# Kernel tuning notes

Measured on AMD Instinct MI355X. Metric: run time of the kernel, lower is better.

## Reference

```python
import jax, jax.numpy as jnp
import numpy as np

B, NI, NO = 4, 256, 256          # batch, num_in, num_out
DIN, DQ, DH, DOUT = 256, 256, 256, 256


def setup_inputs() -> dict:
    key = jax.random.key(0)
    ks = jax.random.split(key, 6)
    def w(k, shape, fan_in):
        return jax.random.normal(k, shape, jnp.float32) / np.sqrt(fan_in).astype(np.float32)
    return {
        "x": jax.random.normal(ks[0], (B, NI, DIN), jnp.float32),
        "query": jax.random.normal(ks[1], (B, NO, DQ), jnp.float32),
        # pre_cond_mlp: Linear(DIN -> DH)
        "W_pre": w(ks[2], (DIN, DH), DIN), "b_pre": jnp.zeros((DH,), jnp.float32),
        # cond_embed: Linear(DQ -> DH)
        "W_emb": w(ks[3], (DQ, DH), DQ), "b_emb": jnp.zeros((DH,), jnp.float32),
        # post_cond_mlp: Linear(2*DH -> DH) + GELU + Linear(DH -> DOUT)
        "W1": w(ks[4], (2 * DH, DH), 2 * DH), "b1": jnp.zeros((DH,), jnp.float32),
        "W2": w(ks[5], (DH, DOUT), DH), "b2": jnp.zeros((DOUT,), jnp.float32),
    }


def reference(x, query, W_pre, b_pre, W_emb, b_emb, W1, b1, W2, b2):
    # pre_cond_mlp(x): [B, NI, DH]
    xp = x @ W_pre + b_pre
    # cond_embed(query): [B, NO, DH]
    c = query @ W_emb + b_emb
    # Original torch code: repeat xp over NO, c over NI, concat -> [B,NI,NO,2*DH],
    # then Linear(2*DH->DH). Algebraically identical (and far cheaper) to split W1
    # and broadcast-add the two projections:
    W1x, W1c = W1[:DH], W1[DH:]          # [DH, DH] each
    h = (xp @ W1x)[:, :, None, :] + (c @ W1c)[:, None, :, :] + b1  # [B, NI, NO, DH]
    h = jax.nn.gelu(h, approximate=False)  # torch nn.GELU default = exact erf
    return h @ W2 + b2                     # [B, NI, NO, DOUT]
```

## Files before the change

### kernel.cpp

```cpp
#include <hip/hip_runtime.h>
#include <hip/hip_bf16.h>
#include <cstdint>
#include <cstddef>


typedef __bf16  bf16x8 __attribute__((ext_vector_type(8)));
typedef float   f32x16 __attribute__((ext_vector_type(16)));

__device__ __forceinline__ float fast_gelu(float x) {
    const float x2 = x * x;
    const float m  = __builtin_fmaf(x2, -0.1029433f, -2.3022072f);
    const float e  = __builtin_amdgcn_exp2f(x * m);
    return x * __builtin_amdgcn_rcpf(1.0f + e);
}

__global__ __launch_bounds__(256) void prep_kernel(
    const float* __restrict__ x, const float* __restrict__ query,
    const float* __restrict__ W_pre, const float* __restrict__ b_pre,
    const float* __restrict__ W_emb, const float* __restrict__ b_emb,
    const float* __restrict__ W1, const float* __restrict__ b1,
    const float* __restrict__ W2,
    float* __restrict__ u, float* __restrict__ v,
    unsigned short* __restrict__ w2t)
{
    const int b = blockIdx.x;
    const int t = threadIdx.x;

    if (b >= 512) {
        const int n0 = (b - 512) * 4;
        const float4 wv = *reinterpret_cast<const float4*>(W2 + (size_t)t * 256 + n0);
        const float vals[4] = {wv.x, wv.y, wv.z, wv.w};
#pragma unroll
        for (int j = 0; j < 4; ++j) {
            const __bf16 bv = (__bf16)vals[j];
            w2t[(size_t)(n0 + j) * 256 + t] = __builtin_bit_cast(unsigned short, bv);
        }
        return;
    }

    const bool isq = (b >= 256);
    const float* __restrict__ A   = isq ? query : x;
    const float* __restrict__ Wa  = isq ? W_emb : W_pre;
    const float* __restrict__ ba  = isq ? b_emb : b_pre;
    const float* __restrict__ W1p = isq ? (W1 + 256 * 256) : W1;
    float* __restrict__ outp      = isq ? v : u;
    const int r0 = (isq ? (b - 256) : b) * 4;

    __shared__ float as[4][256];
    __shared__ float xs[4][256];

#pragma unroll
    for (int r = 0; r < 4; ++r)
        as[r][t] = A[(size_t)(r0 + r) * 256 + t];
    __syncthreads();

    float acc[4] = {0.f, 0.f, 0.f, 0.f};
    {
        float wcur[8];
#pragma unroll
        for (int q = 0; q < 8; ++q) wcur[q] = Wa[(size_t)q * 256 + t];
        for (int k0 = 0; k0 < 248; k0 += 8) {
            float wnxt[8];
#pragma unroll
            for (int q = 0; q < 8; ++q)
                wnxt[q] = Wa[(size_t)(k0 + 8 + q) * 256 + t];
#pragma unroll
            for (int q = 0; q < 8; ++q)
#pragma unroll
                for (int r = 0; r < 4; ++r)
                    acc[r] = __builtin_fmaf(as[r][k0 + q], wcur[q], acc[r]);
#pragma unroll
            for (int q = 0; q < 8; ++q) wcur[q] = wnxt[q];
        }
#pragma unroll
        for (int q = 0; q < 8; ++q)
#pragma unroll
            for (int r = 0; r < 4; ++r)
                acc[r] = __builtin_fmaf(as[r][248 + q], wcur[q], acc[r]);
    }
    const float bav = ba[t];
#pragma unroll
    for (int r = 0; r < 4; ++r) xs[r][t] = acc[r] + bav;
    __syncthreads();

    float acc2[4] = {0.f, 0.f, 0.f, 0.f};
    {
        float wcur[8];
#pragma unroll
        for (int q = 0; q < 8; ++q) wcur[q] = W1p[(size_t)q * 256 + t];
        for (int k0 = 0; k0 < 248; k0 += 8) {
            float wnxt[8];
#pragma unroll
            for (int q = 0; q < 8; ++q)
                wnxt[q] = W1p[(size_t)(k0 + 8 + q) * 256 + t];
#pragma unroll
            for (int q = 0; q < 8; ++q)
#pragma unroll
                for (int r = 0; r < 4; ++r)
                    acc2[r] = __builtin_fmaf(xs[r][k0 + q], wcur[q], acc2[r]);
#pragma unroll
            for (int q = 0; q < 8; ++q) wcur[q] = wnxt[q];
        }
#pragma unroll
        for (int q = 0; q < 8; ++q)
#pragma unroll
            for (int r = 0; r < 4; ++r)
                acc2[r] = __builtin_fmaf(xs[r][248 + q], wcur[q], acc2[r]);
    }
    const float b1v = isq ? 0.f : b1[t];
#pragma unroll
    for (int r = 0; r < 4; ++r)
        outp[(size_t)(r0 + r) * 256 + t] = acc2[r] + b1v;
}

__global__ __launch_bounds__(256, 2) void fused_kernel(
    const float* __restrict__ U, const float* __restrict__ V,
    const unsigned short* __restrict__ W2T, const float* __restrict__ b2,
    float* __restrict__ out)
{
    __shared__ uint4 wlds[2048];
    __shared__ uint4 hlds[1024];
    unsigned int* const hlds32 = reinterpret_cast<unsigned int*>(hlds);

    const int t    = threadIdx.x;
    const int lane = t & 63;
    const int w    = t >> 6;
    const int l31  = lane & 31;
    const int hi   = lane >> 5;

    const size_t r0 = (size_t)blockIdx.x * 128;
    const int bb = (int)(r0 >> 16);
    const int ii = (int)((r0 >> 8) & 255);
    const int j0 = (int)(r0 & 255);

    const float* __restrict__ urow  = U + ((size_t)(bb * 256 + ii)) * 256;
    const float* __restrict__ vbase = V + ((size_t)(bb * 256 + j0)) * 256;

    f32x16 acc[8];
#pragma unroll
    for (int i = 0; i < 8; ++i) acc[i] = (f32x16)0.f;

    for (int kk = 0; kk < 256; kk += 64) {
#pragma unroll
        for (int it = 0; it < 8; ++it) {
            const int idx = it * 256 + t;
            const int n   = idx >> 3;
            const int gp  = idx & 7;
            const int g   = gp ^ (n & 7);
            __builtin_amdgcn_global_load_lds(
                (const __attribute__((address_space(1))) unsigned int*)
                    (W2T + (size_t)n * 256 + kk + g * 8),
                (__attribute__((address_space(3))) unsigned int*)
                    (wlds + idx),
                16, 0, 0);
        }

        const float2 uv2 = *reinterpret_cast<const float2*>(urow + kk + 2 * l31);
        float2 vv[16];
#pragma unroll
        for (int p = 0; p < 16; ++p) {
            const int row = w * 32 + p * 2 + hi;
            vv[p] = *reinterpret_cast<const float2*>(vbase + (size_t)row * 256 + kk + 2 * l31);
        }
#pragma unroll
        for (int p = 0; p < 16; ++p) {
            const int row = w * 32 + p * 2 + hi;
            union { unsigned int u32; __bf16 h[2]; } pk;
            pk.h[0] = (__bf16)fast_gelu(uv2.x + vv[p].x);
            pk.h[1] = (__bf16)fast_gelu(uv2.y + vv[p].y);
            const int d = l31;
            hlds32[row * 32 + (((d >> 2) ^ (row & 7)) << 2) + (d & 3)] = pk.u32;
        }
        __syncthreads();

#pragma unroll
        for (int s = 0; s < 4; ++s) {
            const int gk = 2 * s + hi;
            const int arow = w * 32 + l31;
            const bf16x8 afrag = __builtin_bit_cast(
                bf16x8, hlds[arow * 8 + (gk ^ (arow & 7))]);
#pragma unroll
            for (int cg = 0; cg < 8; ++cg) {
                const int col = cg * 32 + l31;
                const bf16x8 bfrag = __builtin_bit_cast(
                    bf16x8, wlds[col * 8 + (gk ^ (col & 7))]);
                acc[cg] = __builtin_amdgcn_mfma_f32_32x32x16_bf16(
                    afrag, bfrag, acc[cg], 0, 0, 0);
            }
        }
        __syncthreads();
    }

#pragma unroll
    for (int cg = 0; cg < 8; ++cg) {
        const int col = cg * 32 + l31;
        const float bv = b2[col];
#pragma unroll
        for (int rr = 0; rr < 16; ++rr) {
            const int row = w * 32 + 4 * hi + (rr & 3) + 8 * (rr >> 2);
            __builtin_nontemporal_store(acc[cg][rr] + bv,
                                        out + (r0 + row) * 256 + col);
        }
    }
}

extern "C" void kernel_launch(void* const* d_in, const int* in_sizes, int n_in,
                              void* d_out, int out_size, void* d_ws, size_t ws_size,
                              hipStream_t stream)
{
    const float* x     = (const float*)d_in[0];
    const float* query = (const float*)d_in[1];
    const float* W_pre = (const float*)d_in[2];
    const float* b_pre = (const float*)d_in[3];
    const float* W_emb = (const float*)d_in[4];
    const float* b_emb = (const float*)d_in[5];
    const float* W1    = (const float*)d_in[6];
    const float* b1    = (const float*)d_in[7];
    const float* W2    = (const float*)d_in[8];
    const float* b2    = (const float*)d_in[9];
    float* out = (float*)d_out;

    char* ws = (char*)d_ws;
    float* u            = (float*)(ws);
    float* v            = (float*)(ws + (1 << 20));
    unsigned short* w2t = (unsigned short*)(ws + 2 * (1 << 20));

    prep_kernel<<<576, 256, 0, stream>>>(x, query, W_pre, b_pre, W_emb, b_emb,
                                         W1, b1, W2, u, v, w2t);
    fused_kernel<<<2048, 256, 0, stream>>>(u, v, w2t, b2, out);
}
```

Baseline: 105.1 us.

## Keep half of W2 resident in LDS and loop over tasks in persistent blocks

The fused kernel now launches 512 blocks, each owning one 128-column half of W2. That half, covering all K, is loaded into LDS once. Each block then loops over 8 row tiles, with register double-buffering of the U/V loads across K chunks and across tasks. Per-chunk block barriers are dropped because each wave writes and reads only its own rows of the GELU tile. This removes repeated W2 streaming and barrier stalls, but every GELU element is now computed twice (once per column half), LDS use grows, and fewer blocks are resident.

```diff
diff --git a/kernel.cpp b/kernel.cpp
--- a/kernel.cpp
+++ b/kernel.cpp
@@ -118,88 +118,135 @@
     const unsigned short* __restrict__ W2T, const float* __restrict__ b2,
     float* __restrict__ out)
 {
-    __shared__ uint4 wlds[2048];
+    __shared__ uint4 wlds[4096];
     __shared__ uint4 hlds[1024];
-    unsigned int* const hlds32 = reinterpret_cast<unsigned int*>(hlds);
+    unsigned int* const h32 = reinterpret_cast<unsigned int*>(hlds);
 
     const int t    = threadIdx.x;
     const int lane = t & 63;
     const int w    = t >> 6;
     const int l31  = lane & 31;
     const int hi   = lane >> 5;
-
-    const size_t r0 = (size_t)blockIdx.x * 128;
-    const int bb = (int)(r0 >> 16);
-    const int ii = (int)((r0 >> 8) & 255);
-    const int j0 = (int)(r0 & 255);
-
-    const float* __restrict__ urow  = U + ((size_t)(bb * 256 + ii)) * 256;
-    const float* __restrict__ vbase = V + ((size_t)(bb * 256 + j0)) * 256;
-
-    f32x16 acc[8];
-#pragma unroll
-    for (int i = 0; i < 8; ++i) acc[i] = (f32x16)0.f;
-
-    for (int kk = 0; kk < 256; kk += 64) {
-#pragma unroll
-        for (int it = 0; it < 8; ++it) {
-            const int idx = it * 256 + t;
-            const int n   = idx >> 3;
-            const int gp  = idx & 7;
-            const int g   = gp ^ (n & 7);
-            __builtin_amdgcn_global_load_lds(
-                (const __attribute__((address_space(1))) unsigned int*)
-                    (W2T + (size_t)n * 256 + kk + g * 8),
-                (__attribute__((address_space(3))) unsigned int*)
-                    (wlds + idx),
-                16, 0, 0);
-        }
-
-        const float2 uv2 = *reinterpret_cast<const float2*>(urow + kk + 2 * l31);
-        float2 vv[16];
+    const int d    = l31;
+
+    const int bid = blockIdx.x;
+    const int ch  = bid & 1;
+    const int grp = bid >> 1;
+    const int n0  = ch * 128;
+
+#pragma unroll
+    for (int it = 0; it < 16; ++it) {
+        const int idx = it * 256 + t;
+        const int n   = idx >> 5;
+        const int gp  = idx & 31;
+        const int g   = (gp & 24) | ((gp ^ n) & 7);
+        __builtin_amdgcn_global_load_lds(
+            (const __attribute__((address_space(1))) unsigned int*)
+                (W2T + (size_t)(n0 + n) * 256 + g * 8),
+            (__attribute__((address_space(3))) unsigned int*)(wlds + idx),
+            16, 0, 0);
+    }
+
+    float bvv[4];
+#pragma unroll
+    for (int cg = 0; cg < 4; ++cg) bvv[cg] = b2[n0 + cg * 32 + l31];
+
+    float2 vvA[16], vvB[16];
+    float2 u2A, u2B;
+    const float* urow;
+    const float* vrow;
+
+    auto task_ptrs = [&](int task) {
+        const int P    = grp * 8 + task;
+        const int tile = P >> 1;
+        const int jh   = P & 1;
+        const int bb   = tile >> 8;
+        urow = U + (size_t)tile * 256;
+        vrow = V + ((size_t)(bb * 256 + jh * 128)) * 256;
+    };
+
+    auto load_t = [&](int kk, float2& u2, float2 (&vv)[16]) {
+        u2 = *reinterpret_cast<const float2*>(urow + kk + 2 * d);
 #pragma unroll
         for (int p = 0; p < 16; ++p) {
             const int row = w * 32 + p * 2 + hi;
-            vv[p] = *reinterpret_cast<const float2*>(vbase + (size_t)row * 256 + kk + 2 * l31);
-        }
+            vv[p] = *reinterpret_cast<const float2*>(
+                vrow + (size_t)row * 256 + kk + 2 * d);
+        }
+    };
+
+    auto gelu_write = [&](const float2& u2, const float2 (&vv)[16]) {
 #pragma unroll
         for (int p = 0; p < 16; ++p) {
             const int row = w * 32 + p * 2 + hi;
             union { unsigned int u32; __bf16 h[2]; } pk;
-            pk.h[0] = (__bf16)fast_gelu(uv2.x + vv[p].x);
-            pk.h[1] = (__bf16)fast_gelu(uv2.y + vv[p].y);
-            const int d = l31;
-            hlds32[row * 32 + (((d >> 2) ^ (row & 7)) << 2) + (d & 3)] = pk.u32;
-        }
-        __syncthreads();
-
+            pk.h[0] = (__bf16)fast_gelu(u2.x + vv[p].x);
+            pk.h[1] = (__bf16)fast_gelu(u2.y + vv[p].y);
+            h32[row * 32 + (((d >> 2) ^ (row & 7)) << 2) + (d & 3)] = pk.u32;
+        }
+    };
+
+    f32x16 acc[4];
+
+    auto mfma_chunk = [&](int kk) {
+        const int kg0 = kk >> 3;
 #pragma unroll
         for (int s = 0; s < 4; ++s) {
-            const int gk = 2 * s + hi;
+            const int gl   = 2 * s + hi;
             const int arow = w * 32 + l31;
             const bf16x8 afrag = __builtin_bit_cast(
-                bf16x8, hlds[arow * 8 + (gk ^ (arow & 7))]);
-#pragma unroll
-            for (int cg = 0; cg < 8; ++cg) {
-                const int col = cg * 32 + l31;
+                bf16x8, hlds[arow * 8 + (gl ^ (arow & 7))]);
+            const int gk = kg0 + gl;
+#pragma unroll
+            for (int cg = 0; cg < 4; ++cg) {
+                const int nloc = cg * 32 + l31;
+                const int slot = (gk & 24) | ((gk ^ nloc) & 7);
                 const bf16x8 bfrag = __builtin_bit_cast(
-                    bf16x8, wlds[col * 8 + (gk ^ (col & 7))]);
+                    bf16x8, wlds[nloc * 32 + slot]);
                 acc[cg] = __builtin_amdgcn_mfma_f32_32x32x16_bf16(
                     afrag, bfrag, acc[cg], 0, 0, 0);
             }
         }
-        __syncthreads();
-    }
-
-#pragma unroll
-    for (int cg = 0; cg < 8; ++cg) {
-        const int col = cg * 32 + l31;
-        const float bv = b2[col];
-#pragma unroll
-        for (int rr = 0; rr < 16; ++rr) {
-            const int row = w * 32 + 4 * hi + (rr & 3) + 8 * (rr >> 2);
-            __builtin_nontemporal_store(acc[cg][rr] + bv,
-                                        out + (r0 + row) * 256 + col);
+    };
+
+    task_ptrs(0);
+    load_t(0, u2A, vvA);
+
+    __syncthreads();
+
+    for (int task = 0; task < 8; ++task) {
+#pragma unroll
+        for (int i = 0; i < 4; ++i) acc[i] = (f32x16)0.f;
+
+        load_t(64, u2B, vvB);
+        gelu_write(u2A, vvA);
+        mfma_chunk(0);
+        load_t(128, u2A, vvA);
+        gelu_write(u2B, vvB);
+        mfma_chunk(64);
+        load_t(192, u2B, vvB);
+        gelu_write(u2A, vvA);
+        mfma_chunk(128);
+        const int P    = grp * 8 + task;
+        const int tile = P >> 1;
+        const int jh   = P & 1;
+        if (task < 7) {
+            task_ptrs(task + 1);
+            load_t(0, u2A, vvA);
+        }
+        gelu_write(u2B, vvB);
+        mfma_chunk(192);
+
+        const size_t obase = ((size_t)tile << 16) + (size_t)(jh * 128) * 256;
+#pragma unroll
+        for (int cg = 0; cg < 4; ++cg) {
+            const int col = n0 + cg * 32 + l31;
+#pragma unroll
+            for (int rr = 0; rr < 16; ++rr) {
+                const int row = w * 32 + 4 * hi + (rr & 3) + 8 * (rr >> 2);
+                __builtin_nontemporal_store(acc[cg][rr] + bvv[cg],
+                    out + obase + (size_t)row * 256 + col);
+            }
         }
     }
 }
@@ -227,5 +274,5 @@
 
     prep_kernel<<<576, 256, 0, stream>>>(x, query, W_pre, b_pre, W_emb, b_emb,
                                          W1, b1, W2, u, v, w2t);
-    fused_kernel<<<2048, 256, 0, stream>>>(u, v, w2t, b2, out);
-}
+    fused_kernel<<<512, 256, 0, stream>>>(u, v, w2t, b2, out);
+}
```

Result: slower. 112.1 us (+6.7%).

## Use 512-thread blocks with 2x2 wave tiling in fused GEMM kernel

Applied to the files above, without the earlier changes.

Doubles the block to eight waves arranged as a 2x2 grid of 64x64 output sub-tiles. This replaces four waves that each own a 32x256 strip. Each thread holds fewer MFMA accumulators, and the GELU/pack work is split across more threads in two passes. The aim is more resident waves per CU to hide store and load latency. In exchange, A fragments are reused less per B load and each block pays extra barrier cost.

```diff
diff --git a/kernel.cpp b/kernel.cpp
--- a/kernel.cpp
+++ b/kernel.cpp
@@ -113,20 +113,22 @@
         outp[(size_t)(r0 + r) * 256 + t] = acc2[r] + b1v;
 }
 
-__global__ __launch_bounds__(256, 2) void fused_kernel(
+__global__ __launch_bounds__(512, 4) void fused_kernel(
     const float* __restrict__ U, const float* __restrict__ V,
     const unsigned short* __restrict__ W2T, const float* __restrict__ b2,
     float* __restrict__ out)
 {
     __shared__ uint4 wlds[2048];
     __shared__ uint4 hlds[1024];
-    unsigned int* const hlds32 = reinterpret_cast<unsigned int*>(hlds);
+    unsigned int* const h32 = reinterpret_cast<unsigned int*>(hlds);
 
     const int t    = threadIdx.x;
     const int lane = t & 63;
     const int w    = t >> 6;
     const int l31  = lane & 31;
     const int hi   = lane >> 5;
+    const int wr   = w >> 2;
+    const int wc   = w & 3;
 
     const size_t r0 = (size_t)blockIdx.x * 128;
     const int bb = (int)(r0 >> 16);
@@ -136,70 +138,86 @@
     const float* __restrict__ urow  = U + ((size_t)(bb * 256 + ii)) * 256;
     const float* __restrict__ vbase = V + ((size_t)(bb * 256 + j0)) * 256;
 
-    f32x16 acc[8];
-#pragma unroll
-    for (int i = 0; i < 8; ++i) acc[i] = (f32x16)0.f;
+    const int d  = t & 31;
+    const int rb = t >> 5;
+
+    f32x16 acc[2][2];
+#pragma unroll
+    for (int rg = 0; rg < 2; ++rg)
+#pragma unroll
+        for (int cg = 0; cg < 2; ++cg) acc[rg][cg] = (f32x16)0.f;
 
     for (int kk = 0; kk < 256; kk += 64) {
 #pragma unroll
-        for (int it = 0; it < 8; ++it) {
-            const int idx = it * 256 + t;
+        for (int it = 0; it < 4; ++it) {
+            const int idx = it * 512 + t;
             const int n   = idx >> 3;
             const int gp  = idx & 7;
             const int g   = gp ^ (n & 7);
             __builtin_amdgcn_global_load_lds(
                 (const __attribute__((address_space(1))) unsigned int*)
                     (W2T + (size_t)n * 256 + kk + g * 8),
-                (__attribute__((address_space(3))) unsigned int*)
-                    (wlds + idx),
+                (__attribute__((address_space(3))) unsigned int*)(wlds + idx),
                 16, 0, 0);
         }
 
-        const float2 uv2 = *reinterpret_cast<const float2*>(urow + kk + 2 * l31);
-        float2 vv[16];
-#pragma unroll
-        for (int p = 0; p < 16; ++p) {
-            const int row = w * 32 + p * 2 + hi;
-            vv[p] = *reinterpret_cast<const float2*>(vbase + (size_t)row * 256 + kk + 2 * l31);
-        }
-#pragma unroll
-        for (int p = 0; p < 16; ++p) {
-            const int row = w * 32 + p * 2 + hi;
-            union { unsigned int u32; __bf16 h[2]; } pk;
-            pk.h[0] = (__bf16)fast_gelu(uv2.x + vv[p].x);
-            pk.h[1] = (__bf16)fast_gelu(uv2.y + vv[p].y);
-            const int d = l31;
-            hlds32[row * 32 + (((d >> 2) ^ (row & 7)) << 2) + (d & 3)] = pk.u32;
+        const float2 u2 = *reinterpret_cast<const float2*>(urow + kk + 2 * d);
+#pragma unroll 1
+        for (int pass = 0; pass < 2; ++pass) {
+            float2 vv[4];
+#pragma unroll
+            for (int p = 0; p < 4; ++p) {
+                const int row = rb + (pass * 4 + p) * 16;
+                vv[p] = *reinterpret_cast<const float2*>(
+                    vbase + (size_t)row * 256 + kk + 2 * d);
+            }
+#pragma unroll
+            for (int p = 0; p < 4; ++p) {
+                const int row = rb + (pass * 4 + p) * 16;
+                union { unsigned int u32; __bf16 h[2]; } pk;
+                pk.h[0] = (__bf16)fast_gelu(u2.x + vv[p].x);
+                pk.h[1] = (__bf16)fast_gelu(u2.y + vv[p].y);
+                h32[row * 32 + (((d >> 2) ^ (row & 7)) << 2) + (d & 3)] = pk.u32;
+            }
         }
         __syncthreads();
 
 #pragma unroll
         for (int s = 0; s < 4; ++s) {
             const int gk = 2 * s + hi;
-            const int arow = w * 32 + l31;
-            const bf16x8 afrag = __builtin_bit_cast(
-                bf16x8, hlds[arow * 8 + (gk ^ (arow & 7))]);
-#pragma unroll
-            for (int cg = 0; cg < 8; ++cg) {
-                const int col = cg * 32 + l31;
-                const bf16x8 bfrag = __builtin_bit_cast(
+            bf16x8 af[2];
+#pragma unroll
+            for (int rg = 0; rg < 2; ++rg) {
+                const int arow = wr * 64 + rg * 32 + l31;
+                af[rg] = __builtin_bit_cast(
+                    bf16x8, hlds[arow * 8 + (gk ^ (arow & 7))]);
+            }
+#pragma unroll
+            for (int cg = 0; cg < 2; ++cg) {
+                const int col = wc * 64 + cg * 32 + l31;
+                const bf16x8 bf_ = __builtin_bit_cast(
                     bf16x8, wlds[col * 8 + (gk ^ (col & 7))]);
-                acc[cg] = __builtin_amdgcn_mfma_f32_32x32x16_bf16(
-                    afrag, bfrag, acc[cg], 0, 0, 0);
+#pragma unroll
+                for (int rg = 0; rg < 2; ++rg)
+                    acc[rg][cg] = __builtin_amdgcn_mfma_f32_32x32x16_bf16(
+                        af[rg], bf_, acc[rg][cg], 0, 0, 0);
             }
         }
         __syncthreads();
     }
 
 #pragma unroll
-    for (int cg = 0; cg < 8; ++cg) {
-        const int col = cg * 32 + l31;
-        const float bv = b2[col];
-#pragma unroll
-        for (int rr = 0; rr < 16; ++rr) {
-            const int row = w * 32 + 4 * hi + (rr & 3) + 8 * (rr >> 2);
-            __builtin_nontemporal_store(acc[cg][rr] + bv,
-                                        out + (r0 + row) * 256 + col);
+    for (int rg = 0; rg < 2; ++rg) {
+#pragma unroll
+        for (int cg = 0; cg < 2; ++cg) {
+            const int col = wc * 64 + cg * 32 + l31;
+            const float bv = b2[col];
+#pragma unroll
+            for (int rr = 0; rr < 16; ++rr) {
+                const int row = wr * 64 + rg * 32 + 4 * hi + (rr & 3) + 8 * (rr >> 2);
+                __builtin_nontemporal_store(acc[rg][cg][rr] + bv,
+                                            out + (r0 + row) * 256 + col);
+            }
         }
     }
 }
@@ -227,5 +245,5 @@
 
     prep_kernel<<<576, 256, 0, stream>>>(x, query, W_pre, b_pre, W_emb, b_emb,
                                          W1, b1, W2, u, v, w2t);
-    fused_kernel<<<2048, 256, 0, stream>>>(u, v, w2t, b2, out);
-}
+    fused_kernel<<<2048, 512, 0, stream>>>(u, v, w2t, b2, out);
+}
```

Result: faster. 100.8 us (-4.0%).

## Drop LDS staging; build MFMA fragments directly from pre-transposed V and W2 layouts

Applied to the files above, without the earlier changes.

The prep kernel now writes V transposed and W2 in an MFMA-fragment-ready bf16 layout, so the fused kernel can build its A operand in registers from U plus strided V^T loads and read B fragments straight from global memory. This removes the shared-memory staging, swizzling and both barriers per k-step. Every wave now re-reads W2 fragments from global/L2 with no LDS reuse, and the V^T loads are strided per element. Nontemporal output stores are also replaced by plain stores.

```diff
diff --git a/kernel.cpp b/kernel.cpp
--- a/kernel.cpp
+++ b/kernel.cpp
@@ -20,8 +20,8 @@
     const float* __restrict__ W_emb, const float* __restrict__ b_emb,
     const float* __restrict__ W1, const float* __restrict__ b1,
     const float* __restrict__ W2,
-    float* __restrict__ u, float* __restrict__ v,
-    unsigned short* __restrict__ w2t)
+    float* __restrict__ u, float* __restrict__ vt,
+    unsigned short* __restrict__ w2f)
 {
     const int b = blockIdx.x;
     const int t = threadIdx.x;
@@ -30,10 +30,12 @@
         const int n0 = (b - 512) * 4;
         const float4 wv = *reinterpret_cast<const float4*>(W2 + (size_t)t * 256 + n0);
         const float vals[4] = {wv.x, wv.y, wv.z, wv.w};
+        const int g = t >> 3, e = t & 7;
 #pragma unroll
         for (int j = 0; j < 4; ++j) {
             const __bf16 bv = (__bf16)vals[j];
-            w2t[(size_t)(n0 + j) * 256 + t] = __builtin_bit_cast(unsigned short, bv);
+            w2f[((size_t)(g * 256 + n0 + j)) * 8 + e] =
+                __builtin_bit_cast(unsigned short, bv);
         }
         return;
     }
@@ -43,7 +45,6 @@
     const float* __restrict__ Wa  = isq ? W_emb : W_pre;
     const float* __restrict__ ba  = isq ? b_emb : b_pre;
     const float* __restrict__ W1p = isq ? (W1 + 256 * 256) : W1;
-    float* __restrict__ outp      = isq ? v : u;
     const int r0 = (isq ? (b - 256) : b) * 4;
 
     __shared__ float as[4][256];
@@ -107,99 +108,85 @@
             for (int r = 0; r < 4; ++r)
                 acc2[r] = __builtin_fmaf(xs[r][248 + q], wcur[q], acc2[r]);
     }
-    const float b1v = isq ? 0.f : b1[t];
-#pragma unroll
-    for (int r = 0; r < 4; ++r)
-        outp[(size_t)(r0 + r) * 256 + t] = acc2[r] + b1v;
+
+    if (!isq) {
+        const float b1v = b1[t];
+#pragma unroll
+        for (int r = 0; r < 4; ++r)
+            u[(size_t)(r0 + r) * 256 + t] = acc2[r] + b1v;
+    } else {
+        const int bb = r0 >> 8;
+        const int jb = r0 & 255;
+#pragma unroll
+        for (int r = 0; r < 4; ++r)
+            vt[((size_t)(bb * 256 + t)) * 256 + (jb + r)] = acc2[r];
+    }
 }
 
 __global__ __launch_bounds__(256, 2) void fused_kernel(
-    const float* __restrict__ U, const float* __restrict__ V,
-    const unsigned short* __restrict__ W2T, const float* __restrict__ b2,
+    const float* __restrict__ U, const float* __restrict__ VT,
+    const unsigned short* __restrict__ W2F, const float* __restrict__ b2,
     float* __restrict__ out)
 {
-    __shared__ uint4 wlds[2048];
-    __shared__ uint4 hlds[1024];
-    unsigned int* const hlds32 = reinterpret_cast<unsigned int*>(hlds);
-
     const int t    = threadIdx.x;
     const int lane = t & 63;
     const int w    = t >> 6;
     const int l31  = lane & 31;
     const int hi   = lane >> 5;
 
-    const size_t r0 = (size_t)blockIdx.x * 128;
-    const int bb = (int)(r0 >> 16);
-    const int ii = (int)((r0 >> 8) & 255);
-    const int j0 = (int)(r0 & 255);
-
-    const float* __restrict__ urow  = U + ((size_t)(bb * 256 + ii)) * 256;
-    const float* __restrict__ vbase = V + ((size_t)(bb * 256 + j0)) * 256;
+    const int bid  = blockIdx.x;
+    const int tile = bid >> 1;
+    const int jh   = bid & 1;
+    const int bb   = tile >> 8;
+
+    const int jloc = jh * 128 + w * 32 + l31;
+    const float* __restrict__ urow  = U + (size_t)tile * 256;
+    const float* __restrict__ vtcol = VT + ((size_t)(bb * 256)) * 256 + jloc;
 
     f32x16 acc[8];
 #pragma unroll
     for (int i = 0; i < 8; ++i) acc[i] = (f32x16)0.f;
 
-    for (int kk = 0; kk < 256; kk += 64) {
-#pragma unroll
-        for (int it = 0; it < 8; ++it) {
-            const int idx = it * 256 + t;
-            const int n   = idx >> 3;
-            const int gp  = idx & 7;
-            const int g   = gp ^ (n & 7);
-            __builtin_amdgcn_global_load_lds(
-                (const __attribute__((address_space(1))) unsigned int*)
-                    (W2T + (size_t)n * 256 + kk + g * 8),
-                (__attribute__((address_space(3))) unsigned int*)
-                    (wlds + idx),
-                16, 0, 0);
-        }
-
-        const float2 uv2 = *reinterpret_cast<const float2*>(urow + kk + 2 * l31);
-        float2 vv[16];
-#pragma unroll
-        for (int p = 0; p < 16; ++p) {
-            const int row = w * 32 + p * 2 + hi;
-            vv[p] = *reinterpret_cast<const float2*>(vbase + (size_t)row * 256 + kk + 2 * l31);
-        }
-#pragma unroll
-        for (int p = 0; p < 16; ++p) {
-            const int row = w * 32 + p * 2 + hi;
-            union { unsigned int u32; __bf16 h[2]; } pk;
-            pk.h[0] = (__bf16)fast_gelu(uv2.x + vv[p].x);
-            pk.h[1] = (__bf16)fast_gelu(uv2.y + vv[p].y);
-            const int d = l31;
-            hlds32[row * 32 + (((d >> 2) ^ (row & 7)) << 2) + (d & 3)] = pk.u32;
-        }
-        __syncthreads();
-
-#pragma unroll
-        for (int s = 0; s < 4; ++s) {
-            const int gk = 2 * s + hi;
-            const int arow = w * 32 + l31;
-            const bf16x8 afrag = __builtin_bit_cast(
-                bf16x8, hlds[arow * 8 + (gk ^ (arow & 7))]);
-#pragma unroll
-            for (int cg = 0; cg < 8; ++cg) {
-                const int col = cg * 32 + l31;
-                const bf16x8 bfrag = __builtin_bit_cast(
-                    bf16x8, wlds[col * 8 + (gk ^ (col & 7))]);
-                acc[cg] = __builtin_amdgcn_mfma_f32_32x32x16_bf16(
-                    afrag, bfrag, acc[cg], 0, 0, 0);
-            }
-        }
-        __syncthreads();
-    }
-
+#pragma unroll 4
+    for (int s = 0; s < 16; ++s) {
+        const int kb = s * 16 + hi * 8;
+        const float4 ua = *reinterpret_cast<const float4*>(urow + kb);
+        const float4 ub = *reinterpret_cast<const float4*>(urow + kb + 4);
+        float vtv[8];
+#pragma unroll
+        for (int e = 0; e < 8; ++e)
+            vtv[e] = vtcol[(size_t)(kb + e) * 256];
+
+        bf16x8 af;
+        af[0] = (__bf16)fast_gelu(ua.x + vtv[0]);
+        af[1] = (__bf16)fast_gelu(ua.y + vtv[1]);
+        af[2] = (__bf16)fast_gelu(ua.z + vtv[2]);
+        af[3] = (__bf16)fast_gelu(ua.w + vtv[3]);
+        af[4] = (__bf16)fast_gelu(ub.x + vtv[4]);
+        af[5] = (__bf16)fast_gelu(ub.y + vtv[5]);
+        af[6] = (__bf16)fast_gelu(ub.z + vtv[6]);
+        af[7] = (__bf16)fast_gelu(ub.w + vtv[7]);
+
+        const int g = 2 * s + hi;
+#pragma unroll
+        for (int cg = 0; cg < 8; ++cg) {
+            const uint4 braw = *reinterpret_cast<const uint4*>(
+                W2F + ((size_t)(g * 256 + cg * 32 + l31)) * 8);
+            const bf16x8 bf_ = __builtin_bit_cast(bf16x8, braw);
+            acc[cg] = __builtin_amdgcn_mfma_f32_32x32x16_bf16(
+                af, bf_, acc[cg], 0, 0, 0);
+        }
+    }
+
+    const size_t obase = ((size_t)tile << 16) + (size_t)(jh * 128 + w * 32) * 256;
 #pragma unroll
     for (int cg = 0; cg < 8; ++cg) {
         const int col = cg * 32 + l31;
         const float bv = b2[col];
 #pragma unroll
         for (int rr = 0; rr < 16; ++rr) {
-            const int row = w * 32 + 4 * hi + (rr & 3) + 8 * (rr >> 2);
-            __builtin_nontemporal_store(acc[cg][rr] + bv,
-                                        out + (r0 + row) * 256 + col);
+            const int row = 4 * hi + (rr & 3) + 8 * (rr >> 2);
+            out[obase + (size_t)row * 256 + col] = acc[cg][rr] + bv;
         }
     }
 }
@@ -222,10 +209,10 @@
 
     char* ws = (char*)d_ws;
     float* u            = (float*)(ws);
-    float* v            = (float*)(ws + (1 << 20));
-    unsigned short* w2t = (unsigned short*)(ws + 2 * (1 << 20));
+    float* vt           = (float*)(ws + (1 << 20));
+    unsigned short* w2f = (unsigned short*)(ws + 2 * (1 << 20));
 
     prep_kernel<<<576, 256, 0, stream>>>(x, query, W_pre, b_pre, W_emb, b_emb,
-                                         W1, b1, W2, u, v, w2t);
-    fused_kernel<<<2048, 256, 0, stream>>>(u, v, w2t, b2, out);
-}
+                                         W1, b1, W2, u, vt, w2f);
+    fused_kernel<<<2048, 256, 0, stream>>>(u, vt, w2f, b2, out);
+}
```

Result: slower. 157.5 us (+49.9%).
